# Kernel tuning notes

Hardware: AMD Instinct MI355X
Metric: run time of the kernel (lower is better)

Reference implementation:

```python
import jax, jax.numpy as jnp
import numpy as np

HEAD_NUM, HEAD_DIM, HIDDEN = 16, 64, 1024


def setup_inputs() -> dict:
    key = jax.random.key(0)
    ks = jax.random.split(key, 9)
    s = 1.0 / np.sqrt(HIDDEN)
    x = jax.random.normal(ks[0], (4, 2048, HIDDEN), dtype=jnp.float32)
    Wq = jax.random.uniform(ks[1], (HIDDEN, HIDDEN), jnp.float32, -s, s)
    bq = jax.random.uniform(ks[2], (HIDDEN,), jnp.float32, -s, s)
    Wk = jax.random.uniform(ks[3], (HIDDEN, HIDDEN), jnp.float32, -s, s)
    bk = jax.random.uniform(ks[4], (HIDDEN,), jnp.float32, -s, s)
    Wv = jax.random.uniform(ks[5], (HIDDEN, HIDDEN), jnp.float32, -s, s)
    bv = jax.random.uniform(ks[6], (HIDDEN,), jnp.float32, -s, s)
    Wo = jax.random.uniform(ks[7], (HIDDEN, HIDDEN), jnp.float32, -s, s)
    bo = jax.random.uniform(ks[8], (HIDDEN,), jnp.float32, -s, s)
    return {"x": x, "Wq": Wq, "bq": bq, "Wk": Wk, "bk": bk,
            "Wv": Wv, "bv": bv, "Wo": Wo, "bo": bo}


def reference(x, Wq, bq, Wk, bk, Wv, bv, Wo, bo):
    B, S, _ = x.shape
    H, D = HEAD_NUM, HEAD_DIM
    # Linear: x @ W^T + b (torch nn.Linear convention)
    q = (x @ Wq.T + bq).reshape(B, S, H, D).transpose(0, 2, 1, 3)  # [B,H,S,D]
    k = (x @ Wk.T + bk).reshape(B, S, H, D).transpose(0, 2, 1, 3)
    v = (x @ Wv.T + bv).reshape(B, S, H, D).transpose(0, 2, 1, 3)
    scores = jnp.einsum('bhqd,bhkd->bhqk', q, k) / np.sqrt(D)  # [B,H,S,S]
    attn = jax.nn.softmax(scores, axis=-1)  # dropout p=0.0 -> identity
    out = jnp.einsum('bhqk,bhkd->bhqd', attn, v)
    out = out.transpose(0, 2, 1, 3).reshape(B, S, H * D)
    return out @ Wo.T + bo
```

## Files before the change

kernel.cpp:

```cpp
#include <hip/hip_runtime.h>
#include <hip/hip_bf16.h>


typedef __attribute__((ext_vector_type(8))) short short8;
typedef __attribute__((ext_vector_type(4))) short short4b;
typedef __attribute__((ext_vector_type(4))) float floatx4;

#define HID 1024
#define SEQ 2048
#define BATCH 4
#define NH 16
#define HD 64
#define M_TOT (BATCH * SEQ)

#define BM 128
#define BN 128
#define BK 64

#define SCALE2 0.1803368801111204f

typedef const __attribute__((address_space(1))) void g_void;
typedef __attribute__((address_space(3))) void lds_void;

static __device__ __forceinline__ ushort f2bf(float f) {
    union { float f; unsigned int u; } v;
    v.f = f;
    unsigned int u = v.u;
    return (ushort)((u + 0x7fffu + ((u >> 16) & 1u)) >> 16);
}
static __device__ __forceinline__ ushort4 f4tobf(float4 f) {
    ushort4 r;
    r.x = f2bf(f.x); r.y = f2bf(f.y); r.z = f2bf(f.z); r.w = f2bf(f.w);
    return r;
}
static __device__ __forceinline__ unsigned int fbits(float f) {
    union { float f; unsigned int u; } v; v.f = f; return v.u;
}

#define X_F4 (M_TOT * HID / 4)
#define W_F4 (HID * HID / 4)

__global__ __launch_bounds__(256) void convert_bf16(
    const float* __restrict__ x,
    const float* __restrict__ wq, const float* __restrict__ wk,
    const float* __restrict__ wv, const float* __restrict__ wo,
    ushort* __restrict__ xo,
    ushort* __restrict__ wqo, ushort* __restrict__ wko,
    ushort* __restrict__ wvo, ushort* __restrict__ woo)
{
    long i = (long)blockIdx.x * 256 + threadIdx.x;
    const float4* src; ushort4* dst; long off;
    if (i < X_F4)                  { src = (const float4*)x;  dst = (ushort4*)xo;  off = i; }
    else if (i < X_F4 + W_F4)      { src = (const float4*)wq; dst = (ushort4*)wqo; off = i - X_F4; }
    else if (i < X_F4 + 2 * W_F4)  { src = (const float4*)wk; dst = (ushort4*)wko; off = i - X_F4 - W_F4; }
    else if (i < X_F4 + 3 * W_F4)  { src = (const float4*)wv; dst = (ushort4*)wvo; off = i - X_F4 - 2 * W_F4; }
    else                           { src = (const float4*)wo; dst = (ushort4*)woo; off = i - X_F4 - 3 * W_F4; }
    dst[off] = f4tobf(src[off]);
}

template <int MODE>
__global__ __launch_bounds__(256) void gemm_bf(
    const ushort* __restrict__ A,
    const ushort* __restrict__ W0, const ushort* __restrict__ W1,
    const ushort* __restrict__ W2,
    const float* __restrict__ b0, const float* __restrict__ b1,
    const float* __restrict__ b2,
    ushort* __restrict__ o0, ushort* __restrict__ o1, ushort* __restrict__ o2,
    float* __restrict__ of)
{
    __shared__ ushort As[BM * BK];
    __shared__ ushort Bs[BN * BK];

    const int tid  = threadIdx.x;
    const int wave = tid >> 6;
    const int lane = tid & 63;
    const int l16  = lane & 15;
    const int lq   = lane >> 4;

    const int m0 = blockIdx.x * BM;
    const int n0 = blockIdx.y * BN;
    const int z  = (MODE == 1) ? blockIdx.z : 0;

    const ushort* W   = (z == 0) ? W0 : (z == 1) ? W1 : W2;
    const float* bias = (z == 0) ? b0 : (z == 1) ? b1 : b2;

    const int wm = (wave & 1) * 64;
    const int wn = (wave >> 1) * 64;

    const int srow = lane >> 3;
    const int schk = (lane & 7) ^ srow;
    const ushort* gA = A + (size_t)(m0 + wave * 32 + srow) * HID + schk * 8;
    const ushort* gW = W + (size_t)(n0 + wave * 32 + srow) * HID + schk * 8;
    ushort* lA = As + (wave * 32) * BK;
    ushort* lB = Bs + (wave * 32) * BK;

    floatx4 acc[4][4];
#pragma unroll
    for (int i = 0; i < 4; i++)
#pragma unroll
        for (int j = 0; j < 4; j++)
            acc[i][j] = (floatx4){0.f, 0.f, 0.f, 0.f};

    for (int k0 = 0; k0 < HID; k0 += BK) {
        __syncthreads();
#pragma unroll
        for (int i = 0; i < 4; i++) {
            __builtin_amdgcn_global_load_lds(
                (g_void*)(gA + (size_t)(8 * i) * HID + k0),
                (lds_void*)(lA + (8 * i) * BK), 16, 0, 0);
            __builtin_amdgcn_global_load_lds(
                (g_void*)(gW + (size_t)(8 * i) * HID + k0),
                (lds_void*)(lB + (8 * i) * BK), 16, 0, 0);
        }
        __syncthreads();

        const int sw = l16 & 7;
#pragma unroll
        for (int kk8 = 0; kk8 < 8; kk8 += 4) {
            short8 a[4], b[4];
#pragma unroll
            for (int i = 0; i < 4; i++)
                a[i] = *(const short8*)(&As[(wm + i * 16 + l16) * BK + ((lq + kk8) ^ sw) * 8]);
#pragma unroll
            for (int j = 0; j < 4; j++)
                b[j] = *(const short8*)(&Bs[(wn + j * 16 + l16) * BK + ((lq + kk8) ^ sw) * 8]);
#pragma unroll
            for (int i = 0; i < 4; i++)
#pragma unroll
                for (int j = 0; j < 4; j++)
                    acc[i][j] = __builtin_amdgcn_mfma_f32_16x16x32_bf16(
                        a[i], b[j], acc[i][j], 0, 0, 0);
        }
    }

    if (MODE == 0) {
#pragma unroll
        for (int j = 0; j < 4; j++) {
            int n = n0 + wn + j * 16 + l16;
            float bv = bias[n];
#pragma unroll
            for (int i = 0; i < 4; i++)
#pragma unroll
                for (int r = 0; r < 4; r++) {
                    int m = m0 + wm + i * 16 + lq * 4 + r;
                    of[(size_t)m * HID + n] = acc[i][j][r] + bv;
                }
        }
    } else if (z == 1) {
        ushort* out = o1;
#pragma unroll
        for (int j = 0; j < 4; j++) {
            int n = n0 + wn + j * 16 + l16;
            float bv = bias[n];
            int h_ = n >> 6, d_ = n & (HD - 1);
#pragma unroll
            for (int i = 0; i < 4; i++)
#pragma unroll
                for (int r = 0; r < 4; r++) {
                    int m = m0 + wm + i * 16 + lq * 4 + r;
                    int b_ = m >> 11, s_ = m & (SEQ - 1);
                    out[(((size_t)b_ * NH + h_) * SEQ + s_) * HD + d_] =
                        f2bf(acc[i][j][r] + bv);
                }
        }
    } else {
        ushort* out = (z == 0) ? o0 : o2;
        const float sc = (z == 0) ? SCALE2 : 1.0f;
#pragma unroll
        for (int j = 0; j < 4; j++) {
            int n = n0 + wn + j * 16 + l16;
            float bv = bias[n];
            int h_ = n >> 6, d_ = n & (HD - 1);
#pragma unroll
            for (int i = 0; i < 4; i++) {
                int m = m0 + wm + i * 16 + lq * 4;
                int b_ = m >> 11, s0 = m & (SEQ - 1);
                ushort4 pk;
                pk.x = f2bf((acc[i][j][0] + bv) * sc);
                pk.y = f2bf((acc[i][j][1] + bv) * sc);
                pk.z = f2bf((acc[i][j][2] + bv) * sc);
                pk.w = f2bf((acc[i][j][3] + bv) * sc);
                *(ushort4*)(out + (((size_t)b_ * NH + h_) * HD + d_) * SEQ + s0) = pk;
            }
        }
    }
}

__global__ __launch_bounds__(256, 4) void attn_flash(
    const ushort* __restrict__ q, const ushort* __restrict__ k,
    const ushort* __restrict__ v, ushort* __restrict__ o)
{
    __shared__ ushort Ks[2 * 64 * 64];
    __shared__ ushort Vs[2 * 64 * 64];

    const int tid  = threadIdx.x;
    const int wave = tid >> 6;
    const int lane = tid & 63;
    const int l16  = lane & 15;
    const int lq   = lane >> 4;
    const int e    = l16 & 7;

    const int qb = blockIdx.x;
    const int bh = blockIdx.y;
    const int b_ = bh >> 4, h_ = bh & 15;

    const size_t base = (size_t)bh * SEQ * HD;
    const ushort* Qt = q + base;
    const ushort* K  = k + base;
    const ushort* Vt = v + base;

    const int q0 = qb * 64 + wave * 16;

    short8 qf[2];
#pragma unroll
    for (int jj = 0; jj < 8; jj++) {
        qf[0][jj] = (short)Qt[(size_t)(lq * 8 + jj) * SEQ + q0 + l16];
        qf[1][jj] = (short)Qt[(size_t)(32 + lq * 8 + jj) * SEQ + q0 + l16];
    }

    const int srow = lane >> 3;
    const int schk = (lane & 7) ^ srow;
    const ushort* gK = K  + (size_t)(wave * 8 + srow) * HD  + schk * 8;
    const ushort* gV = Vt + (size_t)(wave * 8 + srow) * SEQ + schk * 8;

    floatx4 oacc[4];
#pragma unroll
    for (int jd = 0; jd < 4; jd++) oacc[jd] = (floatx4){0.f, 0.f, 0.f, 0.f};
    float l_ = 0.f;

    const int c0 = lq ^ e;
    const int c1 = (lq + 4) ^ e;

#pragma unroll
    for (int i = 0; i < 2; i++) {
        __builtin_amdgcn_global_load_lds(
            (g_void*)(gK + (size_t)(i * 32) * HD),
            (lds_void*)(Ks + (i * 32 + wave * 8) * 64), 16, 0, 0);
        __builtin_amdgcn_global_load_lds(
            (g_void*)(gV + (size_t)(i * 32) * SEQ),
            (lds_void*)(Vs + (i * 32 + wave * 8) * 64), 16, 0, 0);
    }

    for (int t = 0; t < SEQ / 64; t++) {
        __syncthreads();

        if (t + 1 < SEQ / 64) {
            const int nb = (t + 1) & 1;
#pragma unroll
            for (int i = 0; i < 2; i++) {
                __builtin_amdgcn_global_load_lds(
                    (g_void*)(gK + (size_t)((t + 1) * 64 + i * 32) * HD),
                    (lds_void*)(Ks + nb * 4096 + (i * 32 + wave * 8) * 64), 16, 0, 0);
                __builtin_amdgcn_global_load_lds(
                    (g_void*)(gV + (size_t)(i * 32) * SEQ + (t + 1) * 64),
                    (lds_void*)(Vs + nb * 4096 + (i * 32 + wave * 8) * 64), 16, 0, 0);
            }
        }

        const ushort* Kb = Ks + (t & 1) * 4096;
        const ushort* Vb = Vs + (t & 1) * 4096;

        floatx4 st[4];
#pragma unroll
        for (int j = 0; j < 4; j++) {
            short8 kf0 = *(const short8*)(&Kb[(j * 16 + l16) * 64 + c0 * 8]);
            short8 kf1 = *(const short8*)(&Kb[(j * 16 + l16) * 64 + c1 * 8]);
            floatx4 zz = (floatx4){0.f, 0.f, 0.f, 0.f};
            zz = __builtin_amdgcn_mfma_f32_16x16x32_bf16(kf0, qf[0], zz, 0, 0, 0);
            st[j] = __builtin_amdgcn_mfma_f32_16x16x32_bf16(kf1, qf[1], zz, 0, 0, 0);
        }

        short4b pf[4];
        float rs = 0.f;
#pragma unroll
        for (int j = 0; j < 4; j++) {
            float p0 = __builtin_amdgcn_exp2f(st[j][0]);
            float p1 = __builtin_amdgcn_exp2f(st[j][1]);
            float p2 = __builtin_amdgcn_exp2f(st[j][2]);
            float p3 = __builtin_amdgcn_exp2f(st[j][3]);
            rs += (p0 + p1) + (p2 + p3);
            union { unsigned int u[2]; short4b s; } pk;
            pk.u[0] = __builtin_amdgcn_perm(fbits(p1), fbits(p0), 0x07060302u);
            pk.u[1] = __builtin_amdgcn_perm(fbits(p3), fbits(p2), 0x07060302u);
            pf[j] = pk.s;
        }
        l_ += rs;

#pragma unroll
        for (int j = 0; j < 4; j++) {
#pragma unroll
            for (int jd = 0; jd < 4; jd++) {
                short4b vf = *(const short4b*)(
                    &Vb[(jd * 16 + l16) * 64 + ((2 * j + (lq >> 1)) ^ e) * 8 + (lq & 1) * 4]);
                oacc[jd] = __builtin_amdgcn_mfma_f32_16x16x16bf16_1k(
                    vf, pf[j], oacc[jd], 0, 0, 0);
            }
        }
    }

    l_ += __shfl_xor(l_, 16, 64);
    l_ += __shfl_xor(l_, 32, 64);

    {
        int qg = q0 + l16;
        float invl = 1.0f / l_;
#pragma unroll
        for (int jd = 0; jd < 4; jd++) {
            ushort4 pk;
            pk.x = f2bf(oacc[jd][0] * invl);
            pk.y = f2bf(oacc[jd][1] * invl);
            pk.z = f2bf(oacc[jd][2] * invl);
            pk.w = f2bf(oacc[jd][3] * invl);
            *(ushort4*)(o + ((size_t)b_ * SEQ + qg) * HID + h_ * HD + jd * 16 + lq * 4) = pk;
        }
    }
}

extern "C" void kernel_launch(void* const* d_in, const int* in_sizes, int n_in,
                              void* d_out, int out_size, void* d_ws, size_t ws_size,
                              hipStream_t stream)
{
    const float* x  = (const float*)d_in[0];
    const float* Wq = (const float*)d_in[1];
    const float* bq = (const float*)d_in[2];
    const float* Wk = (const float*)d_in[3];
    const float* bk = (const float*)d_in[4];
    const float* Wv = (const float*)d_in[5];
    const float* bv = (const float*)d_in[6];
    const float* Wo = (const float*)d_in[7];
    const float* bo = (const float*)d_in[8];
    float* out = (float*)d_out;

    const size_t TE = (size_t)M_TOT * HID;
    const size_t WE = (size_t)HID * HID;
    ushort* qws = (ushort*)d_ws;
    ushort* kws = qws + TE;
    ushort* vws = kws + TE;
    ushort* xbf = vws + TE;
    ushort* aws = xbf;
    ushort* wqb = xbf + TE;
    ushort* wkb = wqb + WE;
    ushort* wvb = wkb + WE;
    ushort* wob = wvb + WE;

    convert_bf16<<<(X_F4 + 4 * W_F4) / 256, 256, 0, stream>>>(
        x, Wq, Wk, Wv, Wo, xbf, wqb, wkb, wvb, wob);

    dim3 g1(M_TOT / BM, HID / BN, 3);
    gemm_bf<1><<<g1, 256, 0, stream>>>(xbf, wqb, wkb, wvb, bq, bk, bv,
                                       qws, kws, vws, nullptr);

    dim3 g2(SEQ / 64, BATCH * NH, 1);
    attn_flash<<<g2, 256, 0, stream>>>(qws, kws, vws, aws);

    dim3 g3(M_TOT / BM, HID / BN, 1);
    gemm_bf<0><<<g3, 256, 0, stream>>>(aws, wob, wob, wob, bo, bo, bo,
                                       nullptr, nullptr, nullptr, out);
}
```

Before: 284.5 us.

## Switch flash attention to 32x32x16 MFMA with 128-query blocks

Rewrites the attention inner loop to use 32x32x16 bf16 MFMA instructions instead of 16x16 variants, with each wave handling 32 query rows and each block 128 queries. P fragments are rearranged with cross-half lane shuffles to match the B-operand layout for the PV product. This halves the number of blocks and doubles K/V reuse per LDS tile. In exchange it uses more registers per wave and adds shuffle overhead.

Result: faster. 276.7 us (-2.8%).

```diff
diff --git a/kernel.cpp b/kernel.cpp
--- a/kernel.cpp
+++ b/kernel.cpp
@@ -2,9 +2,9 @@
 #include <hip/hip_bf16.h>
 
 
-typedef __attribute__((ext_vector_type(8))) short short8;
-typedef __attribute__((ext_vector_type(4))) short short4b;
-typedef __attribute__((ext_vector_type(4))) float floatx4;
+typedef __attribute__((ext_vector_type(8)))  short short8;
+typedef __attribute__((ext_vector_type(4)))  float floatx4;
+typedef __attribute__((ext_vector_type(16))) float floatx16;
 
 #define HID 1024
 #define SEQ 2048
@@ -196,9 +196,9 @@
     const int tid  = threadIdx.x;
     const int wave = tid >> 6;
     const int lane = tid & 63;
-    const int l16  = lane & 15;
-    const int lq   = lane >> 4;
-    const int e    = l16 & 7;
+    const int l32  = lane & 31;
+    const int hi   = lane >> 5;
+    const int e    = l32 & 7;
 
     const int qb = blockIdx.x;
     const int bh = blockIdx.y;
@@ -209,27 +209,26 @@
     const ushort* K  = k + base;
     const ushort* Vt = v + base;
 
-    const int q0 = qb * 64 + wave * 16;
-
-    short8 qf[2];
-#pragma unroll
-    for (int jj = 0; jj < 8; jj++) {
-        qf[0][jj] = (short)Qt[(size_t)(lq * 8 + jj) * SEQ + q0 + l16];
-        qf[1][jj] = (short)Qt[(size_t)(32 + lq * 8 + jj) * SEQ + q0 + l16];
-    }
+    const int q0 = qb * 128 + wave * 32;
+
+    short8 qf[4];
+#pragma unroll
+    for (int dk = 0; dk < 4; dk++)
+#pragma unroll
+        for (int jj = 0; jj < 8; jj++)
+            qf[dk][jj] = (short)Qt[(size_t)(dk * 16 + hi * 8 + jj) * SEQ + q0 + l32];
 
     const int srow = lane >> 3;
     const int schk = (lane & 7) ^ srow;
     const ushort* gK = K  + (size_t)(wave * 8 + srow) * HD  + schk * 8;
     const ushort* gV = Vt + (size_t)(wave * 8 + srow) * SEQ + schk * 8;
 
-    floatx4 oacc[4];
-#pragma unroll
-    for (int jd = 0; jd < 4; jd++) oacc[jd] = (floatx4){0.f, 0.f, 0.f, 0.f};
+    floatx16 oacc[2];
+#pragma unroll
+    for (int dm = 0; dm < 2; dm++)
+#pragma unroll
+        for (int r = 0; r < 16; r++) oacc[dm][r] = 0.f;
     float l_ = 0.f;
-
-    const int c0 = lq ^ e;
-    const int c1 = (lq + 4) ^ e;
 
 #pragma unroll
     for (int i = 0; i < 2; i++) {
@@ -260,59 +259,80 @@
         const ushort* Kb = Ks + (t & 1) * 4096;
         const ushort* Vb = Vs + (t & 1) * 4096;
 
-        floatx4 st[4];
-#pragma unroll
-        for (int j = 0; j < 4; j++) {
-            short8 kf0 = *(const short8*)(&Kb[(j * 16 + l16) * 64 + c0 * 8]);
-            short8 kf1 = *(const short8*)(&Kb[(j * 16 + l16) * 64 + c1 * 8]);
-            floatx4 zz = (floatx4){0.f, 0.f, 0.f, 0.f};
-            zz = __builtin_amdgcn_mfma_f32_16x16x32_bf16(kf0, qf[0], zz, 0, 0, 0);
-            st[j] = __builtin_amdgcn_mfma_f32_16x16x32_bf16(kf1, qf[1], zz, 0, 0, 0);
-        }
-
-        short4b pf[4];
+        floatx16 st[2];
+#pragma unroll
+        for (int mt = 0; mt < 2; mt++) {
+#pragma unroll
+            for (int r = 0; r < 16; r++) st[mt][r] = 0.f;
+#pragma unroll
+            for (int dk = 0; dk < 4; dk++) {
+                short8 kf = *(const short8*)(
+                    &Kb[(mt * 32 + l32) * 64 + ((2 * dk + hi) ^ e) * 8]);
+                st[mt] = __builtin_amdgcn_mfma_f32_32x32x16_bf16(
+                    kf, qf[dk], st[mt], 0, 0, 0);
+            }
+        }
+
+        unsigned int P32[2][8];
         float rs = 0.f;
 #pragma unroll
-        for (int j = 0; j < 4; j++) {
-            float p0 = __builtin_amdgcn_exp2f(st[j][0]);
-            float p1 = __builtin_amdgcn_exp2f(st[j][1]);
-            float p2 = __builtin_amdgcn_exp2f(st[j][2]);
-            float p3 = __builtin_amdgcn_exp2f(st[j][3]);
-            rs += (p0 + p1) + (p2 + p3);
-            union { unsigned int u[2]; short4b s; } pk;
-            pk.u[0] = __builtin_amdgcn_perm(fbits(p1), fbits(p0), 0x07060302u);
-            pk.u[1] = __builtin_amdgcn_perm(fbits(p3), fbits(p2), 0x07060302u);
-            pf[j] = pk.s;
+        for (int mt = 0; mt < 2; mt++) {
+            float p[16];
+#pragma unroll
+            for (int r = 0; r < 16; r++) {
+                p[r] = __builtin_amdgcn_exp2f(st[mt][r]);
+                rs += p[r];
+            }
+#pragma unroll
+            for (int rr = 0; rr < 8; rr++)
+                P32[mt][rr] = __builtin_amdgcn_perm(
+                    fbits(p[2 * rr + 1]), fbits(p[2 * rr]), 0x07060302u);
         }
         l_ += rs;
 
 #pragma unroll
-        for (int j = 0; j < 4; j++) {
-#pragma unroll
-            for (int jd = 0; jd < 4; jd++) {
-                short4b vf = *(const short4b*)(
-                    &Vb[(jd * 16 + l16) * 64 + ((2 * j + (lq >> 1)) ^ e) * 8 + (lq & 1) * 4]);
-                oacc[jd] = __builtin_amdgcn_mfma_f32_16x16x16bf16_1k(
-                    vf, pf[j], oacc[jd], 0, 0, 0);
-            }
-        }
-    }
-
-    l_ += __shfl_xor(l_, 16, 64);
+        for (int sc = 0; sc < 4; sc++) {
+            const int mt = sc >> 1;
+            const int bse = 4 * (sc & 1);
+            unsigned int X = P32[mt][bse],     Y = P32[mt][bse + 1];
+            unsigned int Z = P32[mt][bse + 2], W = P32[mt][bse + 3];
+            unsigned int sendA = hi ? X : Z;
+            unsigned int sendB = hi ? Y : W;
+            unsigned int recvA = (unsigned int)__shfl_xor((int)sendA, 32, 64);
+            unsigned int recvB = (unsigned int)__shfl_xor((int)sendB, 32, 64);
+            unsigned int u0 = hi ? recvA : X;
+            unsigned int u1 = hi ? recvB : Y;
+            unsigned int u2 = hi ? Z : recvA;
+            unsigned int u3 = hi ? W : recvB;
+            union { unsigned int u[4]; short8 s; } pfr;
+            pfr.u[0] = u0; pfr.u[1] = u1; pfr.u[2] = u2; pfr.u[3] = u3;
+#pragma unroll
+            for (int dm = 0; dm < 2; dm++) {
+                short8 vf = *(const short8*)(
+                    &Vb[(dm * 32 + l32) * 64 + ((2 * sc + hi) ^ e) * 8]);
+                oacc[dm] = __builtin_amdgcn_mfma_f32_32x32x16_bf16(
+                    vf, pfr.s, oacc[dm], 0, 0, 0);
+            }
+        }
+    }
+
     l_ += __shfl_xor(l_, 32, 64);
 
     {
-        int qg = q0 + l16;
-        float invl = 1.0f / l_;
-#pragma unroll
-        for (int jd = 0; jd < 4; jd++) {
-            ushort4 pk;
-            pk.x = f2bf(oacc[jd][0] * invl);
-            pk.y = f2bf(oacc[jd][1] * invl);
-            pk.z = f2bf(oacc[jd][2] * invl);
-            pk.w = f2bf(oacc[jd][3] * invl);
-            *(ushort4*)(o + ((size_t)b_ * SEQ + qg) * HID + h_ * HD + jd * 16 + lq * 4) = pk;
-        }
+        const int qg = q0 + l32;
+        const float invl = 1.0f / l_;
+#pragma unroll
+        for (int dm = 0; dm < 2; dm++)
+#pragma unroll
+            for (int g = 0; g < 4; g++) {
+                int d0 = dm * 32 + 8 * g + 4 * hi;
+                ushort4 pk;
+                pk.x = f2bf(oacc[dm][4 * g + 0] * invl);
+                pk.y = f2bf(oacc[dm][4 * g + 1] * invl);
+                pk.z = f2bf(oacc[dm][4 * g + 2] * invl);
+                pk.w = f2bf(oacc[dm][4 * g + 3] * invl);
+                *(ushort4*)(o + ((size_t)b_ * SEQ + qg) * HID + h_ * HD + d0) = pk;
+            }
     }
 }
 
@@ -350,7 +370,7 @@
     gemm_bf<1><<<g1, 256, 0, stream>>>(xbf, wqb, wkb, wvb, bq, bk, bv,
                                        qws, kws, vws, nullptr);
 
-    dim3 g2(SEQ / 64, BATCH * NH, 1);
+    dim3 g2(SEQ / 128, BATCH * NH, 1);
     attn_flash<<<g2, 256, 0, stream>>>(qws, kws, vws, aws);
 
     dim3 g3(M_TOT / BM, HID / BN, 1);
```
